# Performance work log

Hardware: AMD Instinct MI355X
Metric: run time of the kernel (lower is better)

The kernel has to match this reference:

```python
import jax, jax.numpy as jnp
import numpy as np
import math

D_K = 64

def setup_inputs() -> dict:
    key = jax.random.key(0)
    ks = jax.random.split(key, 7)
    B, S, d = 8, 2048, D_K
    H = 4096
    Q = jax.random.normal(ks[0], (B, S, d), dtype=jnp.float32)
    K = jax.random.normal(ks[1], (B, S, d), dtype=jnp.float32)
    V = jax.random.normal(ks[2], (B, S, d), dtype=jnp.float32)
    # Linear params (stored as [in, out]); scaled like torch default init
    W1 = jax.random.normal(ks[3], (S, H), dtype=jnp.float32) / math.sqrt(S)
    b1 = jnp.zeros((H,), dtype=jnp.float32)
    W2 = jax.random.normal(ks[4], (H, S), dtype=jnp.float32) / math.sqrt(H)
    b2 = jnp.zeros((S,), dtype=jnp.float32)
    return {"Q": Q, "K": K, "V": V, "W1": W1, "b1": b1, "W2": W2, "b2": b2}

def reference(Q, K, V, W1, b1, W2, b2):
    # scores: [B, Sq, Sk]
    scores = jnp.einsum('bqd,bkd->bqk', Q, K) / jnp.sqrt(jnp.float32(D_K))
    # 2-layer MLP applied along the last (Sk) axis of the scores
    h = jax.nn.relu(jnp.einsum('bqk,kh->bqh', scores, W1) + b1)
    adjusted = jnp.einsum('bqh,hk->bqk', h, W2) + b2
    attn = jax.nn.softmax(adjusted, axis=-1)
    return jnp.einsum('bqk,bkd->bqd', attn, V)
```

## Files before the change

kernel.cpp:

```cpp
#include <hip/hip_runtime.h>
#include <hip/hip_bf16.h>
#include <stdint.h>

#define S 2048
#define D 64
#define H 4096
#define NB 8

typedef __bf16 bf16;
typedef __attribute__((ext_vector_type(8))) __bf16 bf16x8;
typedef __attribute__((ext_vector_type(4))) __bf16 bf16x4;
typedef __attribute__((ext_vector_type(4))) float f32x4;

__device__ __forceinline__ void dma16_raw(const bf16* g, uint32_t m0_bytes) {
  uint32_t m0s = __builtin_amdgcn_readfirstlane(m0_bytes);
  asm volatile("s_mov_b32 m0, %1\n\t"
               "global_load_lds_dwordx4 %0, off"
               :: "v"(g), "s"(m0s) : "memory");
}

__device__ __forceinline__ uint32_t lds_off_bytes(const void* p) {
  return (uint32_t)(uintptr_t)(__attribute__((address_space(3))) const void*)p;
}

__global__ __launch_bounds__(256) void transpose_cast(const float* __restrict__ W,
                                                      bf16* __restrict__ Wt,
                                                      int K, int N) {
  __shared__ float tile[64][65];
  int k0 = blockIdx.y * 64, n0 = blockIdx.x * 64;
  int c = threadIdx.x & 63;
  int r4 = threadIdx.x >> 6;
#pragma unroll
  for (int i = 0; i < 16; ++i) {
    int r = i * 4 + r4;
    tile[r][c] = W[(size_t)(k0 + r) * N + n0 + c];
  }
  __syncthreads();
#pragma unroll
  for (int i = 0; i < 16; ++i) {
    int r = i * 4 + r4;
    Wt[(size_t)(n0 + r) * K + k0 + c] = (bf16)tile[c][r];
  }
}

__global__ __launch_bounds__(256) void vt_cast(const float* __restrict__ V,
                                               bf16* __restrict__ Vt) {
  __shared__ float tile[64][65];
  int z = blockIdx.y;
  int s0 = blockIdx.x * 64;
  const float* Vb = V + (size_t)z * (S * D);
  bf16* Vtb = Vt + (size_t)z * (D * S);
  int c = threadIdx.x & 63;
  int r4 = threadIdx.x >> 6;
#pragma unroll
  for (int i = 0; i < 16; ++i) {
    int r = i * 4 + r4;
    tile[r][c] = Vb[(size_t)(s0 + r) * D + c];
  }
  __syncthreads();
#pragma unroll
  for (int i = 0; i < 16; ++i) {
    int r = i * 4 + r4;
    Vtb[(size_t)r * S + s0 + c] = (bf16)tile[c][r];
  }
}

__global__ __launch_bounds__(256) void cast_bf16(const float* __restrict__ x,
                                                 bf16* __restrict__ y) {
  int i = blockIdx.x * 256 + threadIdx.x;
  f32x4 v = ((const f32x4*)x)[i];
  bf16x4 o;
  o[0] = (bf16)v.x; o[1] = (bf16)v.y; o[2] = (bf16)v.z; o[3] = (bf16)v.w;
  ((bf16x4*)y)[i] = o;
}

template <int RELU, int OUTBF16>
__global__ __launch_bounds__(256, 2) void gemm_bt(const bf16* __restrict__ A,
                                                  const bf16* __restrict__ Bt,
                                                  const float* __restrict__ bias,
                                                  void* __restrict__ Cv,
                                                  float scale,
                                                  int M, int N, int K,
                                                  long strideA, long strideB,
                                                  long strideC) {
  __shared__ __align__(16) bf16 smem[24576];
  int tid = threadIdx.x;
  int lane = tid & 63;
  int w = tid >> 6;

  int m0 = blockIdx.y * 128, n0 = blockIdx.x * 256;
  const bf16* Ab = A + (size_t)blockIdx.z * strideA;
  const bf16* Btb = Bt + (size_t)blockIdx.z * strideB;

  int grow = tid >> 2;
  int gcol = (((lane & 3) ^ ((lane >> 3) & 3)) * 8);
  const bf16* gA0 = Ab + (size_t)(m0 + grow) * K + gcol;
  const bf16* gA1 = gA0 + (size_t)64 * K;
  const bf16* gB0 = Btb + (size_t)(n0 + grow) * K + gcol;
  const bf16* gB1 = gB0 + (size_t)64 * K;
  const bf16* gB2 = gB0 + (size_t)128 * K;
  const bf16* gB3 = gB0 + (size_t)192 * K;

  uint32_t ldsBase = lds_off_bytes(&smem[0]);
  uint32_t wb = (uint32_t)(w * 1024);
  uint32_t mA[2], mB[2];
  mA[0] = ldsBase + wb;          mA[1] = ldsBase + 8192 + wb;
  mB[0] = ldsBase + 16384 + wb;  mB[1] = ldsBase + 32768 + wb;

  int mw = (w & 1) * 64, nw = (w >> 1) * 128;
  int lr = lane & 15;
  int ck = lane >> 4;
  int swz = (ck ^ ((lr >> 1) & 3)) * 8;
  const bf16* paBase = smem + (size_t)(mw + lr) * 32 + swz;
  const bf16* pbBase = smem + 8192 + (size_t)(nw + lr) * 32 + swz;

  f32x4 zero = {0.f, 0.f, 0.f, 0.f};
  f32x4 acc[4][8];
#pragma unroll
  for (int mt = 0; mt < 4; ++mt)
#pragma unroll
    for (int nt = 0; nt < 8; ++nt) acc[mt][nt] = zero;

  const int niter = K / 32;

#define STAGE(buf, koff)                                 \
  do {                                                   \
    dma16_raw(gA0 + (koff), mA[buf]);                    \
    dma16_raw(gA1 + (koff), mA[buf] + 4096);             \
    dma16_raw(gB0 + (koff), mB[buf]);                    \
    dma16_raw(gB1 + (koff), mB[buf] + 4096);             \
    dma16_raw(gB2 + (koff), mB[buf] + 8192);             \
    dma16_raw(gB3 + (koff), mB[buf] + 12288);            \
  } while (0)

  STAGE(0, 0);
  STAGE(1, 32);

  for (int it = 0; it < niter; ++it) {
    int buf = it & 1;
    asm volatile("s_waitcnt vmcnt(6)\n\ts_barrier" ::: "memory");
    const bf16* pa = paBase + buf * 4096;
    const bf16* pb = pbBase + buf * 8192;
    bf16x8 af[4], bfr[8];
#pragma unroll
    for (int mt = 0; mt < 4; ++mt) af[mt] = *(const bf16x8*)(pa + mt * (16 * 32));
#pragma unroll
    for (int nt = 0; nt < 8; ++nt) bfr[nt] = *(const bf16x8*)(pb + nt * (16 * 32));
    asm volatile("s_waitcnt lgkmcnt(0)\n\ts_barrier" ::: "memory");
    int kpre = it + 2 < niter ? (it + 2) * 32 : (niter - 1) * 32;
    STAGE(buf, kpre);
#pragma unroll
    for (int mt = 0; mt < 4; ++mt)
#pragma unroll
      for (int nt = 0; nt < 8; ++nt)
        acc[mt][nt] = __builtin_amdgcn_mfma_f32_16x16x32_bf16(af[mt], bfr[nt],
                                                              acc[mt][nt], 0, 0, 0);
  }
#undef STAGE
  asm volatile("s_waitcnt vmcnt(0)" ::: "memory");

  int mbase = m0 + mw + (lane >> 4) * 4;
  int nbase = n0 + nw + (lane & 15);
#pragma unroll
  for (int mt = 0; mt < 4; ++mt) {
#pragma unroll
    for (int nt = 0; nt < 8; ++nt) {
      int n = nbase + nt * 16;
      float bv = bias ? bias[n] : 0.f;
#pragma unroll
      for (int reg = 0; reg < 4; ++reg) {
        int m = mbase + mt * 16 + reg;
        float v = acc[mt][nt][reg] * scale + bv;
        if (RELU) v = fmaxf(v, 0.f);
        if (OUTBF16) {
          bf16* C = (bf16*)Cv + (size_t)blockIdx.z * strideC;
          C[(size_t)m * N + n] = (bf16)v;
        } else {
          float* C = (float*)Cv + (size_t)blockIdx.z * strideC;
          C[(size_t)m * N + n] = v;
        }
      }
    }
  }
}

template <int RELU, int OUTBF16>
__global__ __launch_bounds__(512, 2) void gemm256(const bf16* __restrict__ A,
                                                  const bf16* __restrict__ Bt,
                                                  const float* __restrict__ bias,
                                                  void* __restrict__ Cv,
                                                  float scale,
                                                  int M, int N, int K,
                                                  long strideA, long strideB,
                                                  long strideC) {
  __shared__ __align__(16) bf16 smem[65536];
  const char* smc = (const char*)&smem[0];

  int tid = threadIdx.x;
  int lane = tid & 63;
  int w = tid >> 6;
  int wm = w >> 2, wn = w & 3;

  unsigned gx = gridDim.x;
  unsigned nwg = gx * gridDim.y;
  unsigned flat = blockIdx.y * gx + blockIdx.x;
  unsigned q = nwg >> 3, r = nwg & 7, xcd = flat & 7, idx = flat >> 3;
  unsigned wg = (xcd < r ? xcd * (q + 1) : r * (q + 1) + (xcd - r) * q) + idx;
  int n0 = (int)(wg % gx) * 256;
  int m0 = (int)(wg / gx) * 256;

  const bf16* Ab = A + (size_t)blockIdx.z * strideA;
  const bf16* Btb = Bt + (size_t)blockIdx.z * strideB;

  int trow = tid >> 3;
  int tg = (tid & 7) ^ (trow & 7);
  const bf16* pgA = Ab + (size_t)(m0 + trow) * K + tg * 8;
  const bf16* pgB = Btb + (size_t)(n0 + trow) * K + tg * 8;
  const size_t s64K = (size_t)K * 64;

  uint32_t ldsBase = lds_off_bytes(&smem[0]);
  uint32_t mb = ldsBase + (uint32_t)(w * 1024);

  int j = lane >> 4, b2 = (lane >> 2) & 1;
  uint32_t rbA0 = (uint32_t)(wm * 8192 + (lane & 15) * 128 +
                             ((j ^ (lane & 3)) * 16) + b2 * 64);
  uint32_t rbA1 = rbA0 ^ 64u;
  uint32_t rbB0 = (uint32_t)(65536 + wn * 4096 + (lane & 15) * 128 +
                             ((j ^ (lane & 3)) * 16) + b2 * 64);
  uint32_t rbB1 = rbB0 ^ 64u;

  f32x4 acc[8][4];
#pragma unroll
  for (int a = 0; a < 8; ++a)
#pragma unroll
    for (int b = 0; b < 2 * 2; ++b) acc[a][b] = (f32x4){0.f, 0.f, 0.f, 0.f};

  bf16x8 af[4][2];
  bf16x8 bf0[2][2];
  bf16x8 bf1[2][2];

#define STG_A(PI, HH, LL, KC) \
  dma16_raw(pgA + (size_t)(2 * (HH) + (LL)) * s64K + (KC), \
            mb + (PI) * 32768 + (HH) * 16384 + (LL) * 8192)
#define STG_B(PI, HH, LL, KC) \
  dma16_raw(pgB + (size_t)(2 * (HH) + (LL)) * s64K + (KC), \
            mb + 65536 + (PI) * 32768 + (HH) * 16384 + (LL) * 8192)
#define STAGE_AH(PI, HH, KC) do { STG_A(PI, HH, 0, KC); STG_A(PI, HH, 1, KC); } while (0)
#define STAGE_BH(PI, HH, KC) do { STG_B(PI, HH, 0, KC); STG_B(PI, HH, 1, KC); } while (0)

#define RDA(PI, QA)                                                            \
  do {                                                                        \
    _Pragma("unroll") for (int mt = 0; mt < 4; ++mt) {                        \
      af[mt][0] = *(const bf16x8*)(smc + rbA0 + ((PI) * 32768 + (QA) * 16384 + mt * 2048)); \
      af[mt][1] = *(const bf16x8*)(smc + rbA1 + ((PI) * 32768 + (QA) * 16384 + mt * 2048)); \
    }                                                                         \
  } while (0)
#define RDB(PI, QB, BF)                                                        \
  do {                                                                        \
    _Pragma("unroll") for (int nt = 0; nt < 2; ++nt) {                        \
      BF[nt][0] = *(const bf16x8*)(smc + rbB0 + ((PI) * 32768 + (QB) * 16384 + nt * 2048)); \
      BF[nt][1] = *(const bf16x8*)(smc + rbB1 + ((PI) * 32768 + (QB) * 16384 + nt * 2048)); \
    }                                                                         \
  } while (0)

#define MFMA_Q(QA, QB, BF)                                                     \
  do {                                                                        \
    __builtin_amdgcn_s_setprio(1);                                            \
    _Pragma("unroll") for (int mt = 0; mt < 4; ++mt)                          \
      _Pragma("unroll") for (int nt = 0; nt < 2; ++nt) {                      \
        f32x4 c = acc[(QA) * 4 + mt][(QB) * 2 + nt];                          \
        c = __builtin_amdgcn_mfma_f32_16x16x32_bf16(af[mt][0], BF[nt][0], c, 0, 0, 0); \
        c = __builtin_amdgcn_mfma_f32_16x16x32_bf16(af[mt][1], BF[nt][1], c, 0, 0, 0); \
        acc[(QA) * 4 + mt][(QB) * 2 + nt] = c;                                \
      }                                                                       \
    __builtin_amdgcn_s_setprio(0);                                            \
  } while (0)

#define BAR() asm volatile("s_barrier" ::: "memory")
#define VMC4() asm volatile("s_waitcnt vmcnt(4)" ::: "memory")

#define TILE2(PI, TT)                                              \
  do {                                                             \
    int c1 = ((TT) + 1 < NT ? (TT) + 1 : NT - 1) * 64;             \
    int c2 = ((TT) + 2 < NT ? (TT) + 2 : NT - 1) * 64;             \
                                                           \
    MFMA_Q(0, 0, bf0);                                             \
    RDB(PI, 1, bf1);                                               \
    STAGE_BH((PI) ^ 1, 0, c1);                                     \
    BAR();                                                         \
                                                           \
    MFMA_Q(0, 1, bf1);                                             \
    RDA(PI, 1);                                                    \
    STAGE_AH(PI, 0, c2);                                           \
    BAR();                                                         \
      \
    STAGE_BH(PI, 1, c2);                                           \
    MFMA_Q(1, 1, bf1);                                             \
    VMC4();                                                        \
    BAR();                                                         \
           \
    MFMA_Q(1, 0, bf0);                                             \
    if ((TT) + 1 < NT) {                                           \
      RDA((PI) ^ 1, 0);                                            \
      RDB((PI) ^ 1, 0, bf0);                                       \
      STAGE_AH(PI, 1, c2);                                         \
      BAR();                                                       \
    }                                                              \
  } while (0)

  STAGE_AH(0, 0, 0);
  STAGE_BH(0, 1, 0);
  STAGE_AH(0, 1, 0);
  STAGE_BH(0, 0, 0);
  STAGE_AH(1, 0, 64);
  STAGE_BH(1, 1, 64);
  asm volatile("s_waitcnt vmcnt(4)\n\ts_barrier" ::: "memory");

  const int NT = K / 64;

  RDA(0, 0);
  RDB(0, 0, bf0);
  STAGE_AH(1, 1, 64);
  BAR();

  for (int T = 0; T < NT; T += 2) {
    TILE2(0, T);
    TILE2(1, T + 1);
  }
#undef TILE2
#undef VMC4
#undef BAR
#undef MFMA_Q
#undef RDB
#undef RDA
#undef STAGE_BH
#undef STAGE_AH
#undef STG_B
#undef STG_A

  asm volatile("s_waitcnt vmcnt(0)" ::: "memory");

  int rowb = m0 + wm * 64 + ((lane >> 4) << 2);
  int colb = n0 + wn * 32 + (lane & 15);
#pragma unroll
  for (int fn = 0; fn < 4; ++fn) {
    int n = colb + (fn >> 1) * 128 + (fn & 1) * 16;
    float bv = bias ? bias[n] : 0.f;
#pragma unroll
    for (int fm = 0; fm < 8; ++fm) {
      int mrow = rowb + (fm >> 2) * 128 + (fm & 3) * 16;
#pragma unroll
      for (int reg = 0; reg < 4; ++reg) {
        float v = acc[fm][fn][reg] * scale + bv;
        if (RELU) v = fmaxf(v, 0.f);
        int m = mrow + reg;
        if (OUTBF16) {
          bf16* C = (bf16*)Cv + (size_t)blockIdx.z * strideC;
          C[(size_t)m * N + n] = (bf16)v;
        } else {
          float* C = (float*)Cv + (size_t)blockIdx.z * strideC;
          C[(size_t)m * N + n] = v;
        }
      }
    }
  }
}

__global__ __launch_bounds__(256) void smav(const float* __restrict__ adj,
                                            const bf16* __restrict__ Vt,
                                            float* __restrict__ out,
                                            long adjStride) {
  int z = blockIdx.y;
  const float* adjb = adj + (size_t)z * adjStride;
  const bf16* Vtb = Vt + (size_t)z * (D * S);
  float* outb = out + (size_t)z * (S * D);
  int q0 = blockIdx.x * 16;
  __shared__ __align__(16) bf16 P[16 * 2048];
  __shared__ float rsum[16];
  int tid = threadIdx.x, w = tid >> 6, lane = tid & 63;
  char* Pc = (char*)&P[0];

#pragma unroll
  for (int i = 0; i < 4; ++i) {
    int r = w * 4 + i;
    const float* rowp = adjb + (size_t)(q0 + r) * S + lane * 4;
    f32x4 rv[8];
    float lm = -1e30f;
#pragma unroll
    for (int kk = 0; kk < 8; ++kk) {
      rv[kk] = *(const f32x4*)(rowp + kk * 256);
      lm = fmaxf(lm, fmaxf(fmaxf(rv[kk].x, rv[kk].y), fmaxf(rv[kk].z, rv[kk].w)));
    }
#pragma unroll
    for (int off = 32; off > 0; off >>= 1) lm = fmaxf(lm, __shfl_xor(lm, off));
    float s = 0.f;
    uint32_t wbase = (uint32_t)(r * 4096 + (lane & 1) * 8);
#pragma unroll
    for (int kk = 0; kk < 8; ++kk) {
      bf16x4 pb;
      pb[0] = (bf16)__expf(rv[kk].x - lm);
      pb[1] = (bf16)__expf(rv[kk].y - lm);
      pb[2] = (bf16)__expf(rv[kk].z - lm);
      pb[3] = (bf16)__expf(rv[kk].w - lm);
      s += (float)pb[0] + (float)pb[1] + (float)pb[2] + (float)pb[3];
      uint32_t g = (uint32_t)(lane >> 1) + (uint32_t)(kk * 32);
      uint32_t gs = g ^ (uint32_t)(r & 7);
      *(bf16x4*)(Pc + wbase + gs * 16) = pb;
    }
#pragma unroll
    for (int off = 32; off > 0; off >>= 1) s += __shfl_xor(s, off);
    if (lane == 0) rsum[r] = s;
  }
  __syncthreads();

  int dl = (w << 4) + (lane & 15);
  const bf16* vrow = Vtb + (size_t)dl * S + (lane >> 4) * 8;
  uint32_t rl = (uint32_t)(lane & 15);
  uint32_t abase = rl * 4096;
  uint32_t rx = rl & 7;
  f32x4 acc0 = {0.f, 0.f, 0.f, 0.f}, acc1 = {0.f, 0.f, 0.f, 0.f};
#pragma unroll 4
  for (int k0 = 0; k0 < S; k0 += 64) {
    uint32_t g0 = (uint32_t)(k0 >> 3) + (uint32_t)(lane >> 4);
    bf16x8 a0 = *(const bf16x8*)(Pc + abase + ((g0 ^ rx) * 16));
    bf16x8 b0 = *(const bf16x8*)(vrow + k0);
    acc0 = __builtin_amdgcn_mfma_f32_16x16x32_bf16(a0, b0, acc0, 0, 0, 0);
    uint32_t g1 = g0 + 4;
    bf16x8 a1 = *(const bf16x8*)(Pc + abase + ((g1 ^ rx) * 16));
    bf16x8 b1 = *(const bf16x8*)(vrow + k0 + 32);
    acc1 = __builtin_amdgcn_mfma_f32_16x16x32_bf16(a1, b1, acc1, 0, 0, 0);
  }
  f32x4 accs = acc0 + acc1;
#pragma unroll
  for (int reg = 0; reg < 4; ++reg) {
    int m = ((lane >> 4) << 2) + reg;
    outb[(size_t)(q0 + m) * D + dl] = accs[reg] / rsum[m];
  }
}

extern "C" void kernel_launch(void* const* d_in, const int* in_sizes, int n_in,
                              void* d_out, int out_size, void* d_ws, size_t ws_size,
                              hipStream_t stream) {
  const float* Q  = (const float*)d_in[0];
  const float* Km = (const float*)d_in[1];
  const float* V  = (const float*)d_in[2];
  const float* W1 = (const float*)d_in[3];
  const float* b1 = (const float*)d_in[4];
  const float* W2 = (const float*)d_in[5];
  const float* b2 = (const float*)d_in[6];
  float* out = (float*)d_out;
  char* ws = (char*)d_ws;

  bf16* W1t  = (bf16*)ws;
  bf16* W2t  = (bf16*)(ws + 16777216);
  bf16* Qb16 = (bf16*)(ws + 33554432);
  bf16* Kb16 = (bf16*)(ws + 35651584);

  transpose_cast<<<dim3(H / 64, S / 64), 256, 0, stream>>>(W1, W1t, S, H);
  transpose_cast<<<dim3(S / 64, H / 64), 256, 0, stream>>>(W2, W2t, H, S);
  cast_bf16<<<dim3(NB * S * D / 1024), 256, 0, stream>>>(Q, Qb16);
  cast_bf16<<<dim3(NB * S * D / 1024), 256, 0, stream>>>(Km, Kb16);

  int G = 1;
  if (ws_size >= 306184192ULL) G = 8;
  else if (ws_size >= 171966464ULL) G = 4;
  else if (ws_size >= 104857600ULL) G = 2;

  bf16* Sc   = (bf16*)(ws + 37748736);
  float* adj = (float*)(ws + 37748736);
  bf16* h    = (bf16*)(ws + 37748736 + (size_t)G * 16777216);
  bf16* Vt   = h;

  for (int b0 = 0; b0 < NB; b0 += G) {
    gemm_bt<0, 1><<<dim3(S / 256, S / 128, G), 256, 0, stream>>>(
        Qb16 + (size_t)b0 * S * D, Kb16 + (size_t)b0 * S * D, nullptr, Sc,
        0.125f, S, S, D, (long)S * D, (long)S * D, (long)S * S);
    gemm256<1, 1><<<dim3(H / 256, S / 256, G), 512, 0, stream>>>(
        Sc, W1t, b1, h, 1.0f, S, H, S, (long)S * S, 0L, (long)S * H);
    gemm256<0, 0><<<dim3(S / 256, S / 256, G), 512, 0, stream>>>(
        h, W2t, b2, adj, 1.0f, S, S, H, (long)S * H, 0L, (long)S * S);
    vt_cast<<<dim3(S / 64, G), 256, 0, stream>>>(V + (size_t)b0 * S * D, Vt);
    smav<<<dim3(S / 16, G), 256, 0, stream>>>(
        adj, Vt, out + (size_t)b0 * S * D, (long)S * S);
  }
}
```

Baseline: 644.2 us.

## Add reworked-schedule GEMM for second MLP layer and vectorize transpose-cast kernels

Adds a new 256x256 GEMM variant used for the h·W2 layer. It reads fragments from LDS in four quarter steps, each followed by a barrier, an lgkmcnt(0) wait and a sched_barrier, so each MFMA quadrant is cleanly separated from the LDS reads and DMA staging. It also vectorizes the W and V transpose-cast kernels to use float4 loads and bf16x4 stores. The extra barriers and waits could reduce overlap between LDS reads and MFMA work compared with the previous interleaved schedule.

```diff
diff --git a/kernel.cpp b/kernel.cpp
--- a/kernel.cpp
+++ b/kernel.cpp
@@ -28,18 +28,23 @@
                                                       int K, int N) {
   __shared__ float tile[64][65];
   int k0 = blockIdx.y * 64, n0 = blockIdx.x * 64;
-  int c = threadIdx.x & 63;
-  int r4 = threadIdx.x >> 6;
-#pragma unroll
-  for (int i = 0; i < 16; ++i) {
-    int r = i * 4 + r4;
-    tile[r][c] = W[(size_t)(k0 + r) * N + n0 + c];
+  int c4 = (threadIdx.x & 15) * 4;
+  int r16 = threadIdx.x >> 4;
+#pragma unroll
+  for (int i = 0; i < 4; ++i) {
+    int r = i * 16 + r16;
+    f32x4 v = *(const f32x4*)&W[(size_t)(k0 + r) * N + n0 + c4];
+    tile[r][c4 + 0] = v.x; tile[r][c4 + 1] = v.y;
+    tile[r][c4 + 2] = v.z; tile[r][c4 + 3] = v.w;
   }
   __syncthreads();
 #pragma unroll
-  for (int i = 0; i < 16; ++i) {
-    int r = i * 4 + r4;
-    Wt[(size_t)(n0 + r) * K + k0 + c] = (bf16)tile[c][r];
+  for (int i = 0; i < 4; ++i) {
+    int n = i * 16 + r16;
+    bf16x4 o;
+    o[0] = (bf16)tile[c4 + 0][n]; o[1] = (bf16)tile[c4 + 1][n];
+    o[2] = (bf16)tile[c4 + 2][n]; o[3] = (bf16)tile[c4 + 3][n];
+    *(bf16x4*)&Wt[(size_t)(n0 + n) * K + k0 + c4] = o;
   }
 }
 
@@ -50,18 +55,23 @@
   int s0 = blockIdx.x * 64;
   const float* Vb = V + (size_t)z * (S * D);
   bf16* Vtb = Vt + (size_t)z * (D * S);
-  int c = threadIdx.x & 63;
-  int r4 = threadIdx.x >> 6;
-#pragma unroll
-  for (int i = 0; i < 16; ++i) {
-    int r = i * 4 + r4;
-    tile[r][c] = Vb[(size_t)(s0 + r) * D + c];
+  int c4 = (threadIdx.x & 15) * 4;
+  int r16 = threadIdx.x >> 4;
+#pragma unroll
+  for (int i = 0; i < 4; ++i) {
+    int r = i * 16 + r16;
+    f32x4 v = *(const f32x4*)&Vb[(size_t)(s0 + r) * D + c4];
+    tile[r][c4 + 0] = v.x; tile[r][c4 + 1] = v.y;
+    tile[r][c4 + 2] = v.z; tile[r][c4 + 3] = v.w;
   }
   __syncthreads();
 #pragma unroll
-  for (int i = 0; i < 16; ++i) {
-    int r = i * 4 + r4;
-    Vtb[(size_t)r * S + s0 + c] = (bf16)tile[c][r];
+  for (int i = 0; i < 4; ++i) {
+    int n = i * 16 + r16;
+    bf16x4 o;
+    o[0] = (bf16)tile[c4 + 0][n]; o[1] = (bf16)tile[c4 + 1][n];
+    o[2] = (bf16)tile[c4 + 2][n]; o[3] = (bf16)tile[c4 + 3][n];
+    *(bf16x4*)&Vtb[(size_t)n * S + s0 + c4] = o;
   }
 }
 
@@ -283,22 +293,18 @@
   do {                                                             \
     int c1 = ((TT) + 1 < NT ? (TT) + 1 : NT - 1) * 64;             \
     int c2 = ((TT) + 2 < NT ? (TT) + 2 : NT - 1) * 64;             \
-                                                           \
     MFMA_Q(0, 0, bf0);                                             \
     RDB(PI, 1, bf1);                                               \
     STAGE_BH((PI) ^ 1, 0, c1);                                     \
     BAR();                                                         \
-                                                           \
     MFMA_Q(0, 1, bf1);                                             \
     RDA(PI, 1);                                                    \
     STAGE_AH(PI, 0, c2);                                           \
     BAR();                                                         \
-      \
     STAGE_BH(PI, 1, c2);                                           \
     MFMA_Q(1, 1, bf1);                                             \
     VMC4();                                                        \
     BAR();                                                         \
-           \
     MFMA_Q(1, 0, bf0);                                             \
     if ((TT) + 1 < NT) {                                           \
       RDA((PI) ^ 1, 0);                                            \
@@ -329,6 +335,172 @@
   }
 #undef TILE2
 #undef VMC4
+#undef BAR
+#undef MFMA_Q
+#undef RDB
+#undef RDA
+#undef STAGE_BH
+#undef STAGE_AH
+#undef STG_B
+#undef STG_A
+
+  asm volatile("s_waitcnt vmcnt(0)" ::: "memory");
+
+  int rowb = m0 + wm * 64 + ((lane >> 4) << 2);
+  int colb = n0 + wn * 32 + (lane & 15);
+#pragma unroll
+  for (int fn = 0; fn < 4; ++fn) {
+    int n = colb + (fn >> 1) * 128 + (fn & 1) * 16;
+    float bv = bias ? bias[n] : 0.f;
+#pragma unroll
+    for (int fm = 0; fm < 8; ++fm) {
+      int mrow = rowb + (fm >> 2) * 128 + (fm & 3) * 16;
+#pragma unroll
+      for (int reg = 0; reg < 4; ++reg) {
+        float v = acc[fm][fn][reg] * scale + bv;
+        if (RELU) v = fmaxf(v, 0.f);
+        int m = mrow + reg;
+        if (OUTBF16) {
+          bf16* C = (bf16*)Cv + (size_t)blockIdx.z * strideC;
+          C[(size_t)m * N + n] = (bf16)v;
+        } else {
+          float* C = (float*)Cv + (size_t)blockIdx.z * strideC;
+          C[(size_t)m * N + n] = v;
+        }
+      }
+    }
+  }
+}
+
+template <int RELU, int OUTBF16>
+__global__ __launch_bounds__(512, 2) void gemm256_v3(const bf16* __restrict__ A,
+                                                     const bf16* __restrict__ Bt,
+                                                     const float* __restrict__ bias,
+                                                     void* __restrict__ Cv,
+                                                     float scale,
+                                                     int M, int N, int K,
+                                                     long strideA, long strideB,
+                                                     long strideC) {
+  __shared__ __align__(16) bf16 smem[65536];
+  const char* smc = (const char*)&smem[0];
+
+  int tid = threadIdx.x;
+  int lane = tid & 63;
+  int w = tid >> 6;
+  int wm = w >> 2, wn = w & 3;
+
+  unsigned gx = gridDim.x;
+  unsigned nwg = gx * gridDim.y;
+  unsigned flat = blockIdx.y * gx + blockIdx.x;
+  unsigned q = nwg >> 3, r = nwg & 7, xcd = flat & 7, idx = flat >> 3;
+  unsigned wg = (xcd < r ? xcd * (q + 1) : r * (q + 1) + (xcd - r) * q) + idx;
+  int n0 = (int)(wg % gx) * 256;
+  int m0 = (int)(wg / gx) * 256;
+
+  const bf16* Ab = A + (size_t)blockIdx.z * strideA;
+  const bf16* Btb = Bt + (size_t)blockIdx.z * strideB;
+
+  int trow = tid >> 3;
+  int tg = (tid & 7) ^ (trow & 7);
+  const bf16* pgA = Ab + (size_t)(m0 + trow) * K + tg * 8;
+  const bf16* pgB = Btb + (size_t)(n0 + trow) * K + tg * 8;
+  const size_t s64K = (size_t)K * 64;
+
+  uint32_t ldsBase = lds_off_bytes(&smem[0]);
+  uint32_t mb = ldsBase + (uint32_t)(w * 1024);
+
+  int j = lane >> 4, b2 = (lane >> 2) & 1;
+  uint32_t rbA0 = (uint32_t)(wm * 8192 + (lane & 15) * 128 +
+                             ((j ^ (lane & 3)) * 16) + b2 * 64);
+  uint32_t rbA1 = rbA0 ^ 64u;
+  uint32_t rbB0 = (uint32_t)(65536 + wn * 4096 + (lane & 15) * 128 +
+                             ((j ^ (lane & 3)) * 16) + b2 * 64);
+  uint32_t rbB1 = rbB0 ^ 64u;
+
+  f32x4 acc[8][4];
+#pragma unroll
+  for (int a = 0; a < 8; ++a)
+#pragma unroll
+    for (int b = 0; b < 2 * 2; ++b) acc[a][b] = (f32x4){0.f, 0.f, 0.f, 0.f};
+
+  bf16x8 af[4][2];
+  bf16x8 bfr[2][2];
+
+#define STG_A(PI, HH, LL, KC) \
+  dma16_raw(pgA + (size_t)(2 * (HH) + (LL)) * s64K + (KC), \
+            mb + (PI) * 32768 + (HH) * 16384 + (LL) * 8192)
+#define STG_B(PI, HH, LL, KC) \
+  dma16_raw(pgB + (size_t)(2 * (HH) + (LL)) * s64K + (KC), \
+            mb + 65536 + (PI) * 32768 + (HH) * 16384 + (LL) * 8192)
+#define STAGE_AH(PI, HH, KC) do { STG_A(PI, HH, 0, KC); STG_A(PI, HH, 1, KC); } while (0)
+#define STAGE_BH(PI, HH, KC) do { STG_B(PI, HH, 0, KC); STG_B(PI, HH, 1, KC); } while (0)
+
+#define RDA(PI, QA)                                                            \
+  do {                                                                        \
+    _Pragma("unroll") for (int mt = 0; mt < 4; ++mt) {                        \
+      af[mt][0] = *(const bf16x8*)(smc + rbA0 + ((PI) * 32768 + (QA) * 16384 + mt * 2048)); \
+      af[mt][1] = *(const bf16x8*)(smc + rbA1 + ((PI) * 32768 + (QA) * 16384 + mt * 2048)); \
+    }                                                                         \
+  } while (0)
+#define RDB(PI, QB)                                                            \
+  do {                                                                        \
+    _Pragma("unroll") for (int nt = 0; nt < 2; ++nt) {                        \
+      bfr[nt][0] = *(const bf16x8*)(smc + rbB0 + ((PI) * 32768 + (QB) * 16384 + nt * 2048)); \
+      bfr[nt][1] = *(const bf16x8*)(smc + rbB1 + ((PI) * 32768 + (QB) * 16384 + nt * 2048)); \
+    }                                                                         \
+  } while (0)
+
+#define MFMA_Q(QA, QB)                                                         \
+  do {                                                                        \
+    __builtin_amdgcn_s_setprio(1);                                            \
+    _Pragma("unroll") for (int mt = 0; mt < 4; ++mt)                          \
+      _Pragma("unroll") for (int nt = 0; nt < 2; ++nt) {                      \
+        f32x4 c = acc[(QA) * 4 + mt][(QB) * 2 + nt];                          \
+        c = __builtin_amdgcn_mfma_f32_16x16x32_bf16(af[mt][0], bfr[nt][0], c, 0, 0, 0); \
+        c = __builtin_amdgcn_mfma_f32_16x16x32_bf16(af[mt][1], bfr[nt][1], c, 0, 0, 0); \
+        acc[(QA) * 4 + mt][(QB) * 2 + nt] = c;                                \
+      }                                                                       \
+    __builtin_amdgcn_s_setprio(0);                                            \
+  } while (0)
+
+#define BAR() asm volatile("s_barrier" ::: "memory")
+#define LGK0SB()                                            \
+  do {                                                      \
+    asm volatile("s_waitcnt lgkmcnt(0)" ::: "memory");      \
+    __builtin_amdgcn_sched_barrier(0);                      \
+  } while (0)
+#define VMC4() asm volatile("s_waitcnt vmcnt(4)" ::: "memory")
+
+#define TILE3(PI, TT)                                              \
+  do {                                                             \
+    int c1 = ((TT) + 1 < NT ? (TT) + 1 : NT - 1) * 64;             \
+    int c2 = ((TT) + 2 < NT ? (TT) + 2 : NT - 1) * 64;             \
+    RDA(PI, 0); RDB(PI, 0); STAGE_AH((PI) ^ 1, 1, c1);             \
+    BAR(); LGK0SB(); MFMA_Q(0, 0); BAR();                          \
+    RDB(PI, 1); STAGE_BH((PI) ^ 1, 0, c1);                         \
+    BAR(); LGK0SB(); MFMA_Q(0, 1); BAR();                          \
+    RDA(PI, 1); STAGE_AH(PI, 0, c2);                               \
+    BAR(); LGK0SB(); MFMA_Q(1, 1); BAR();                          \
+    RDB(PI, 0); STAGE_BH(PI, 1, c2);                               \
+    BAR(); LGK0SB(); MFMA_Q(1, 0); VMC4(); BAR();                  \
+  } while (0)
+
+  STAGE_AH(0, 0, 0);
+  STAGE_BH(0, 1, 0);
+  STAGE_AH(0, 1, 0);
+  STAGE_BH(0, 0, 0);
+  STAGE_AH(1, 0, 64);
+  STAGE_BH(1, 1, 64);
+  asm volatile("s_waitcnt vmcnt(4)\n\ts_barrier" ::: "memory");
+
+  const int NT = K / 64;
+  for (int T = 0; T < NT; T += 2) {
+    TILE3(0, T);
+    TILE3(1, T + 1);
+  }
+#undef TILE3
+#undef VMC4
+#undef LGK0SB
 #undef BAR
 #undef MFMA_Q
 #undef RDB
@@ -477,7 +649,7 @@
         0.125f, S, S, D, (long)S * D, (long)S * D, (long)S * S);
     gemm256<1, 1><<<dim3(H / 256, S / 256, G), 512, 0, stream>>>(
         Sc, W1t, b1, h, 1.0f, S, H, S, (long)S * S, 0L, (long)S * H);
-    gemm256<0, 0><<<dim3(S / 256, S / 256, G), 512, 0, stream>>>(
+    gemm256_v3<0, 0><<<dim3(S / 256, S / 256, G), 512, 0, stream>>>(
         h, W2t, b2, adj, 1.0f, S, S, H, (long)S * H, 0L, (long)S * S);
     vt_cast<<<dim3(S / 64, G), 256, 0, stream>>>(V + (size_t)b0 * S * D, Vt);
     smav<<<dim3(S / 16, G), 256, 0, stream>>>(
```

Measured after the change: 676.7 us. +5.0%, slower.
